# Kernel tuning notes

Measured on AMD Instinct MI355X. Metric: run time of the kernel, lower is better.

The kernel has to match this reference:

```python
import jax, jax.numpy as jnp
import numpy as np

B, Q, K, D = 64, 2048, 2048, 128
NEG = -1e9


def setup_inputs() -> dict:
    key = jax.random.key(0)
    kq, kk, kv, kl = jax.random.split(key, 4)
    return {
        "queries": jax.random.normal(kq, (B, Q, D), dtype=jnp.float32),
        "keys": jax.random.normal(kk, (B, K, D), dtype=jnp.float32),
        "values": jax.random.normal(kv, (B, K, D), dtype=jnp.float32),
        "valid_lens": jax.random.randint(kl, (B,), 0, K, dtype=jnp.int32),
    }


def reference(queries, keys, values, valid_lens):
    d = queries.shape[-1]
    # [B, Q, K] scores
    scores = jnp.einsum("bqd,bkd->bqk", queries, keys) / jnp.sqrt(jnp.float32(d))
    # padding mask: position >= valid_len  (mask_softmax valid_lens path)
    positions = jnp.arange(scores.shape[-1], dtype=valid_lens.dtype)
    pad_mask = positions[None, None, :] >= valid_lens[:, None, None]  # [B,1,K] -> bcast over Q
    scores = jnp.where(pad_mask, jnp.float32(NEG), scores)
    attn = jax.nn.softmax(scores, axis=-1)
    out = jnp.einsum("bqk,bkd->bqd", attn, values)  # dropout p=0.0 -> identity
    return (out, attn)
```

## Files before the change

kernel.cpp:

```cpp
#include <hip/hip_runtime.h>
#include <hip/hip_bf16.h>

#define B_N   64
#define Q_N   2048
#define K_N   2048
#define D_N   128
#define NEGV  (-1e9f)
#define SCALE 0.08838834764831845f

using f32x4  = __attribute__((ext_vector_type(4))) float;
using bf16x8 = __attribute__((ext_vector_type(8))) short;

static __device__ __forceinline__ short tobf(float f) {
  __hip_bfloat16 h = __float2bfloat16(f);
  return __builtin_bit_cast(short, h);
}

__global__ __launch_bounds__(256, 2)
void attn_fused(const float* __restrict__ Qg, const float* __restrict__ Kg,
                const float* __restrict__ Vg, const int* __restrict__ vlg,
                float* __restrict__ outp, float* __restrict__ attnp)
{
  __shared__ __align__(16) short Kst[64 * 136];
  __shared__ __align__(16) short Pt [64 * 68];

  const int id   = blockIdx.x;
  const int xcd  = id & 7;
  const int rest = id >> 3;
  const int b    = (rest >> 5) * 8 + xcd;
  const int q0   = (rest & 31) * 64;

  const int tid  = threadIdx.x;
  const int w    = tid >> 6;
  const int lane = tid & 63;
  const int m16  = lane & 15;
  const int quad = lane >> 4;

  const int vlen = vlg[b];

  const float* Qb = Qg + (size_t)b * Q_N * D_N;
  const float* Kb = Kg + (size_t)b * K_N * D_N;
  const float* Vb = Vg + (size_t)b * K_N * D_N;

  bf16x8 aQ[4];
  {
    const float* qr = Qb + (size_t)(q0 + w*16 + m16) * D_N + quad*8;
    #pragma unroll
    for (int d0 = 0; d0 < 4; ++d0) {
      float4 f0 = *(const float4*)(qr + d0*32);
      float4 f1 = *(const float4*)(qr + d0*32 + 4);
      bf16x8 a;
      a[0]=tobf(f0.x); a[1]=tobf(f0.y); a[2]=tobf(f0.z); a[3]=tobf(f0.w);
      a[4]=tobf(f1.x); a[5]=tobf(f1.y); a[6]=tobf(f1.z); a[7]=tobf(f1.w);
      aQ[d0] = a;
    }
  }

  auto stage_K = [&](int k0) {
    #pragma unroll
    for (int i = 0; i < 4; ++i) {
      int c   = i*256 + tid;
      int row = c >> 4;
      int col = (c & 15) << 3;
      const float* src = Kb + (size_t)(k0 + row) * D_N + col;
      float4 f0 = *(const float4*)(src);
      float4 f1 = *(const float4*)(src + 4);
      bf16x8 v;
      v[0]=tobf(f0.x); v[1]=tobf(f0.y); v[2]=tobf(f0.z); v[3]=tobf(f0.w);
      v[4]=tobf(f1.x); v[5]=tobf(f1.y); v[6]=tobf(f1.z); v[7]=tobf(f1.w);
      *(bf16x8*)&Kst[row*136 + col] = v;
    }
  };

  #define QMAX(v) { v = fmaxf(v, __shfl_xor(v, 1)); v = fmaxf(v, __shfl_xor(v, 2)); \
                    v = fmaxf(v, __shfl_xor(v, 4)); v = fmaxf(v, __shfl_xor(v, 8)); }
  #define QSUM(v) { v += __shfl_xor(v, 1); v += __shfl_xor(v, 2); \
                    v += __shfl_xor(v, 4); v += __shfl_xor(v, 8); }

  float m_r[4], l_r[4];
  #pragma unroll
  for (int r = 0; r < 4; ++r) { m_r[r] = -INFINITY; l_r[r] = 0.0f; }

  for (int k0 = 0; k0 < K_N; k0 += 64) {
    __syncthreads();
    stage_K(k0);
    __syncthreads();
    #pragma unroll
    for (int kt = 0; kt < 4; ++kt) {
      f32x4 acc = {0.f, 0.f, 0.f, 0.f};
      #pragma unroll
      for (int d0 = 0; d0 < 4; ++d0) {
        bf16x8 bk = *(const bf16x8*)&Kst[(kt*16 + m16)*136 + d0*32 + quad*8];
        acc = __builtin_amdgcn_mfma_f32_16x16x32_bf16(aQ[d0], bk, acc, 0, 0, 0);
      }
      const int key = k0 + kt*16 + m16;
      const bool msk = key >= vlen;
      #pragma unroll
      for (int r = 0; r < 4; ++r) {
        float s  = msk ? NEGV : acc[r] * SCALE;
        float rm = s; QMAX(rm);
        float mn = fmaxf(m_r[r], rm);
        float p  = __expf(s - mn);
        QSUM(p);
        l_r[r] = l_r[r] * __expf(m_r[r] - mn) + p;
        m_r[r] = mn;
      }
    }
  }
  float inv_l[4];
  #pragma unroll
  for (int r = 0; r < 4; ++r) inv_l[r] = 1.0f / l_r[r];

  f32x4 accO[4][2];
  #pragma unroll
  for (int mt = 0; mt < 4; ++mt)
    #pragma unroll
    for (int nt = 0; nt < 2; ++nt)
      accO[mt][nt] = (f32x4){0.f, 0.f, 0.f, 0.f};

  for (int k0 = 0; k0 < K_N; k0 += 64) {
    __syncthreads();
    stage_K(k0);
    __syncthreads();

    #pragma unroll
    for (int kt = 0; kt < 4; ++kt) {
      f32x4 acc = {0.f, 0.f, 0.f, 0.f};
      #pragma unroll
      for (int d0 = 0; d0 < 4; ++d0) {
        bf16x8 bk = *(const bf16x8*)&Kst[(kt*16 + m16)*136 + d0*32 + quad*8];
        acc = __builtin_amdgcn_mfma_f32_16x16x32_bf16(aQ[d0], bk, acc, 0, 0, 0);
      }
      const int key = k0 + kt*16 + m16;
      const bool msk = key >= vlen;
      float pv[4];
      #pragma unroll
      for (int r = 0; r < 4; ++r) {
        float s = msk ? NEGV : acc[r] * SCALE;
        pv[r] = __expf(s - m_r[r]) * inv_l[r];
      }
      float* ap = attnp + ((size_t)b * Q_N + q0 + w*16 + quad*4) * K_N + key;
      #pragma unroll
      for (int r = 0; r < 4; ++r)
        __builtin_nontemporal_store(pv[r], ap + (size_t)r * K_N);
      short4 pk = make_short4(tobf(pv[0]), tobf(pv[1]), tobf(pv[2]), tobf(pv[3]));
      *(short4*)&Pt[(kt*16 + m16)*68 + w*16 + quad*4] = pk;
    }
    __syncthreads();

    #pragma unroll
    for (int c = 0; c < 2; ++c) {
      bf16x8 aP[4];
      #pragma unroll
      for (int mt = 0; mt < 4; ++mt) {
        bf16x8 a;
        #pragma unroll
        for (int j = 0; j < 8; ++j)
          a[j] = Pt[(c*32 + quad*8 + j)*68 + mt*16 + m16];
        aP[mt] = a;
      }
      #pragma unroll
      for (int nt = 0; nt < 2; ++nt) {
        const float* vp = Vb + (size_t)(k0 + c*32 + quad*8) * D_N + w*32 + nt*16 + m16;
        bf16x8 bv;
        #pragma unroll
        for (int j = 0; j < 8; ++j) bv[j] = tobf(vp[(size_t)j * D_N]);
        #pragma unroll
        for (int mt = 0; mt < 4; ++mt)
          accO[mt][nt] = __builtin_amdgcn_mfma_f32_16x16x32_bf16(aP[mt], bv, accO[mt][nt], 0, 0, 0);
      }
    }
  }

  #pragma unroll
  for (int mt = 0; mt < 4; ++mt)
    #pragma unroll
    for (int nt = 0; nt < 2; ++nt)
      #pragma unroll
      for (int r = 0; r < 4; ++r) {
        int row = q0 + mt*16 + quad*4 + r;
        int col = w*32 + nt*16 + m16;
        __builtin_nontemporal_store(accO[mt][nt][r],
                                    outp + ((size_t)b * Q_N + row) * D_N + col);
      }
}

extern "C" void kernel_launch(void* const* d_in, const int* in_sizes, int n_in,
                              void* d_out, int out_size, void* d_ws, size_t ws_size,
                              hipStream_t stream) {
  const float* Q  = (const float*)d_in[0];
  const float* K  = (const float*)d_in[1];
  const float* V  = (const float*)d_in[2];
  const int*   vl = (const int*)d_in[3];
  float* outp  = (float*)d_out;
  float* attnp = outp + (size_t)B_N * Q_N * D_N;

  dim3 grid(B_N * (Q_N / 64));
  dim3 block(256);
  hipLaunchKernelGGL(attn_fused, grid, block, 0, stream, Q, K, V, vl, outp, attnp);
}
```

Baseline: 1.887 ms.

## Skip fully masked key tiles, stage V through LDS, batch softmax per tile

Limits both key loops to the valid length rounded up to 64 and writes zeros straight into the masked tail of the attention matrix, skipping QK and PV work on fully padded tiles. V is now converted to bf16 once and staged in shared memory instead of being read from global memory with strided scalar loads. The first pass also computes all four score subtiles before a single max/sum reduction, so there are fewer cross-lane shuffles. When vlen is 0 the full range is still processed, which keeps the uniform-softmax semantics, at the cost of more shared memory and lower possible occupancy.

```diff
diff --git a/kernel.cpp b/kernel.cpp
--- a/kernel.cpp
+++ b/kernel.cpp
@@ -22,6 +22,7 @@
                 float* __restrict__ outp, float* __restrict__ attnp)
 {
   __shared__ __align__(16) short Kst[64 * 136];
+  __shared__ __align__(16) short Vst[64 * 136];
   __shared__ __align__(16) short Pt [64 * 68];
 
   const int id   = blockIdx.x;
@@ -37,10 +38,18 @@
   const int quad = lane >> 4;
 
   const int vlen = vlg[b];
+  const int kT   = (vlen == 0) ? K_N : ((vlen + 63) & ~63);
 
   const float* Qb = Qg + (size_t)b * Q_N * D_N;
   const float* Kb = Kg + (size_t)b * K_N * D_N;
   const float* Vb = Vg + (size_t)b * K_N * D_N;
+
+  {
+    float* arow = attnp + ((size_t)b * Q_N + q0 + (tid >> 2)) * K_N;
+    const f32x4 z = {0.f, 0.f, 0.f, 0.f};
+    for (int col = kT + (tid & 3) * 4; col < K_N; col += 16)
+      __builtin_nontemporal_store(z, (f32x4*)(arow + col));
+  }
 
   bf16x8 aQ[4];
   {
@@ -56,19 +65,19 @@
     }
   }
 
-  auto stage_K = [&](int k0) {
+  auto stage64x128 = [&](const float* __restrict__ srcB, int k0, short* dst) {
     #pragma unroll
     for (int i = 0; i < 4; ++i) {
       int c   = i*256 + tid;
       int row = c >> 4;
       int col = (c & 15) << 3;
-      const float* src = Kb + (size_t)(k0 + row) * D_N + col;
+      const float* src = srcB + (size_t)(k0 + row) * D_N + col;
       float4 f0 = *(const float4*)(src);
       float4 f1 = *(const float4*)(src + 4);
       bf16x8 v;
       v[0]=tobf(f0.x); v[1]=tobf(f0.y); v[2]=tobf(f0.z); v[3]=tobf(f0.w);
       v[4]=tobf(f1.x); v[5]=tobf(f1.y); v[6]=tobf(f1.z); v[7]=tobf(f1.w);
-      *(bf16x8*)&Kst[row*136 + col] = v;
+      *(bf16x8*)&dst[row*136 + col] = v;
     }
   };
 
@@ -81,30 +90,40 @@
   #pragma unroll
   for (int r = 0; r < 4; ++r) { m_r[r] = -INFINITY; l_r[r] = 0.0f; }
 
-  for (int k0 = 0; k0 < K_N; k0 += 64) {
-    __syncthreads();
-    stage_K(k0);
-    __syncthreads();
-    #pragma unroll
-    for (int kt = 0; kt < 4; ++kt) {
-      f32x4 acc = {0.f, 0.f, 0.f, 0.f};
+  for (int k0 = 0; k0 < kT; k0 += 64) {
+    __syncthreads();
+    stage64x128(Kb, k0, Kst);
+    __syncthreads();
+
+    f32x4 acc[4];
+    #pragma unroll
+    for (int kt = 0; kt < 4; ++kt) acc[kt] = (f32x4){0.f,0.f,0.f,0.f};
+    #pragma unroll
+    for (int kt = 0; kt < 4; ++kt)
       #pragma unroll
       for (int d0 = 0; d0 < 4; ++d0) {
         bf16x8 bk = *(const bf16x8*)&Kst[(kt*16 + m16)*136 + d0*32 + quad*8];
-        acc = __builtin_amdgcn_mfma_f32_16x16x32_bf16(aQ[d0], bk, acc, 0, 0, 0);
-      }
-      const int key = k0 + kt*16 + m16;
-      const bool msk = key >= vlen;
-      #pragma unroll
-      for (int r = 0; r < 4; ++r) {
-        float s  = msk ? NEGV : acc[r] * SCALE;
-        float rm = s; QMAX(rm);
-        float mn = fmaxf(m_r[r], rm);
-        float p  = __expf(s - mn);
-        QSUM(p);
-        l_r[r] = l_r[r] * __expf(m_r[r] - mn) + p;
-        m_r[r] = mn;
-      }
+        acc[kt] = __builtin_amdgcn_mfma_f32_16x16x32_bf16(aQ[d0], bk, acc[kt], 0, 0, 0);
+      }
+
+    const int key0 = k0 + m16;
+    const bool mk0 = (key0     ) >= vlen;
+    const bool mk1 = (key0 + 16) >= vlen;
+    const bool mk2 = (key0 + 32) >= vlen;
+    const bool mk3 = (key0 + 48) >= vlen;
+    #pragma unroll
+    for (int r = 0; r < 4; ++r) {
+      float s0 = mk0 ? NEGV : acc[0][r] * SCALE;
+      float s1 = mk1 ? NEGV : acc[1][r] * SCALE;
+      float s2 = mk2 ? NEGV : acc[2][r] * SCALE;
+      float s3 = mk3 ? NEGV : acc[3][r] * SCALE;
+      float tm = fmaxf(fmaxf(s0, s1), fmaxf(s2, s3));
+      QMAX(tm);
+      float mn = fmaxf(m_r[r], tm);
+      float p  = __expf(s0 - mn) + __expf(s1 - mn) + __expf(s2 - mn) + __expf(s3 - mn);
+      QSUM(p);
+      l_r[r] = l_r[r] * __expf(m_r[r] - mn) + p;
+      m_r[r] = mn;
     }
   }
   float inv_l[4];
@@ -118,25 +137,31 @@
     for (int nt = 0; nt < 2; ++nt)
       accO[mt][nt] = (f32x4){0.f, 0.f, 0.f, 0.f};
 
-  for (int k0 = 0; k0 < K_N; k0 += 64) {
-    __syncthreads();
-    stage_K(k0);
-    __syncthreads();
-
-    #pragma unroll
-    for (int kt = 0; kt < 4; ++kt) {
-      f32x4 acc = {0.f, 0.f, 0.f, 0.f};
+  for (int k0 = 0; k0 < kT; k0 += 64) {
+    __syncthreads();
+    stage64x128(Kb, k0, Kst);
+    stage64x128(Vb, k0, Vst);
+    __syncthreads();
+
+    f32x4 acc[4];
+    #pragma unroll
+    for (int kt = 0; kt < 4; ++kt) acc[kt] = (f32x4){0.f,0.f,0.f,0.f};
+    #pragma unroll
+    for (int kt = 0; kt < 4; ++kt)
       #pragma unroll
       for (int d0 = 0; d0 < 4; ++d0) {
         bf16x8 bk = *(const bf16x8*)&Kst[(kt*16 + m16)*136 + d0*32 + quad*8];
-        acc = __builtin_amdgcn_mfma_f32_16x16x32_bf16(aQ[d0], bk, acc, 0, 0, 0);
-      }
+        acc[kt] = __builtin_amdgcn_mfma_f32_16x16x32_bf16(aQ[d0], bk, acc[kt], 0, 0, 0);
+      }
+
+    #pragma unroll
+    for (int kt = 0; kt < 4; ++kt) {
       const int key = k0 + kt*16 + m16;
       const bool msk = key >= vlen;
       float pv[4];
       #pragma unroll
       for (int r = 0; r < 4; ++r) {
-        float s = msk ? NEGV : acc[r] * SCALE;
+        float s = msk ? NEGV : acc[kt][r] * SCALE;
         pv[r] = __expf(s - m_r[r]) * inv_l[r];
       }
       float* ap = attnp + ((size_t)b * Q_N + q0 + w*16 + quad*4) * K_N + key;
@@ -161,10 +186,10 @@
       }
       #pragma unroll
       for (int nt = 0; nt < 2; ++nt) {
-        const float* vp = Vb + (size_t)(k0 + c*32 + quad*8) * D_N + w*32 + nt*16 + m16;
+        const int vcol = w*32 + nt*16 + m16;
         bf16x8 bv;
         #pragma unroll
-        for (int j = 0; j < 8; ++j) bv[j] = tobf(vp[(size_t)j * D_N]);
+        for (int j = 0; j < 8; ++j) bv[j] = Vst[(c*32 + quad*8 + j)*136 + vcol];
         #pragma unroll
         for (int mt = 0; mt < 4; ++mt)
           accO[mt][nt] = __builtin_amdgcn_mfma_f32_16x16x32_bf16(aP[mt], bv, accO[mt][nt], 0, 0, 0);
```

Result: faster. 1.724 ms (-8.6%).
